# Optimization experiments

Hardware: AMD Instinct MI355X
Metric: run time of the kernel (lower is better)

## Reference

```python
import jax, jax.numpy as jnp
import numpy as np

NUM_LANDMARKS = 1024  # must equal seq_len for the source einsum/pinv shapes to be consistent


def setup_inputs() -> dict:
    key = jax.random.key(0)
    ks = jax.random.split(key, 9)
    B, S, D = 4, 1024, 768
    s = 1.0 / np.sqrt(D)  # ~torch Linear default init scale
    return {
        "q": jax.random.normal(ks[0], (B, S, D), jnp.float32),
        "k": jax.random.normal(ks[1], (B, S, D), jnp.float32),
        "v": jax.random.normal(ks[2], (B, S, D), jnp.float32),
        "Wq": jax.random.normal(ks[3], (D, D), jnp.float32) * s,
        "bq": jax.random.normal(ks[4], (D,), jnp.float32) * s,
        "Wk": jax.random.normal(ks[5], (D, D), jnp.float32) * s,
        "bk": jax.random.normal(ks[6], (D,), jnp.float32) * s,
        "Wv": jax.random.normal(ks[7], (D, D), jnp.float32) * s,
        "bv": jax.random.normal(ks[8], (D,), jnp.float32) * s,
    }


def reference(q, k, v, Wq, bq, Wk, bk, Wv, bv):
    B, S, D = q.shape
    m = NUM_LANDMARKS
    # projections + row softmax over feature dim (as in source; note: self.scale is unused there)
    qp = jax.nn.softmax(q @ Wq + bq, axis=-1)            # [B,S,D]
    kp = jax.nn.softmax(k @ Wk + bk, axis=-1)            # [B,S,D]
    vp = v @ Wv + bv                                     # [B,S,D]
    # landmark mean pooling (with m == S this is the identity pooling)
    q_land = qp.reshape(B, m, -1, D).mean(axis=-2)       # [B,m,D]
    k_land = kp.reshape(B, m, -1, D).mean(axis=-2)       # [B,m,D]
    kernel_1 = jnp.einsum('bqd,bkd->bqk', qp, k_land)    # [B,S,m]
    kernel_2 = jnp.einsum('bkd,bld->bkl', k_land, kp)    # [B,m,S]
    kernel_3 = kp * vp                                   # [B,S,D]
    kernel_2_inv = jnp.linalg.pinv(kernel_2)             # [B,S,m] (== [B,m,S] since m==S)
    out = jnp.einsum('bqk,bkl,bld->bqd', kernel_1, kernel_2_inv, kernel_3)
    return out
```

## Files before the change

### kernel.cpp

```cpp
#include <hip/hip_runtime.h>
#include <cstdint>


#define NB 4
#define SS 1024
#define DD 768

static const long PB = (long)SS * DD;
static const long GB = (long)DD * DD;
static const long SZ_P = (long)NB * PB;
static const long SZ_G = (long)NB * GB;

__global__ __launch_bounds__(256)
void gemm_f32(int M, int N, int K,
              const float* __restrict__ A, long sA,
              const float* __restrict__ Bm, long sB,
              float* __restrict__ C, long sC,
              const float* __restrict__ Dm, long sD,
              const float* __restrict__ bias,
              float alpha, float beta)
{
    const int b = blockIdx.z;
    const float* Ab = A + (long)b * sA;
    const float* Bb = Bm + (long)b * sB;
    float*       Cb = C + (long)b * sC;
    const float* Db = Dm ? (Dm + (long)b * sD) : nullptr;

    __shared__ float As[16][68];
    __shared__ float Bs[16][68];

    const int tid = threadIdx.x;
    const int tx = tid & 15, ty = tid >> 4;
    const int row0 = blockIdx.y * 64, col0 = blockIdx.x * 64;

    const int lar = tid >> 2;
    const int lak = (tid & 3) << 2;
    const int lbc = (tid & 15) << 2;
    const int lbk = tid >> 4;

    float acc[4][4] = {};

    for (int k0 = 0; k0 < K; k0 += 16) {
        float4 av = *(const float4*)(Ab + (long)(row0 + lar) * K + (k0 + lak));
        float4 bv = *(const float4*)(Bb + (long)(k0 + lbk) * N + (col0 + lbc));
        As[lak + 0][lar] = av.x;
        As[lak + 1][lar] = av.y;
        As[lak + 2][lar] = av.z;
        As[lak + 3][lar] = av.w;
        *(float4*)(&Bs[lbk][lbc]) = bv;
        __syncthreads();
#pragma unroll
        for (int kk = 0; kk < 16; ++kk) {
            float4 a4 = *(const float4*)(&As[kk][ty << 2]);
            float4 b4 = *(const float4*)(&Bs[kk][tx << 2]);
            float ar[4] = {a4.x, a4.y, a4.z, a4.w};
            float br[4] = {b4.x, b4.y, b4.z, b4.w};
#pragma unroll
            for (int i = 0; i < 4; ++i)
#pragma unroll
                for (int j = 0; j < 4; ++j)
                    acc[i][j] = fmaf(ar[i], br[j], acc[i][j]);
        }
        __syncthreads();
    }

#pragma unroll
    for (int i = 0; i < 4; ++i) {
        const int r = row0 + (ty << 2) + i;
#pragma unroll
        for (int j = 0; j < 4; ++j) {
            const int c = col0 + (tx << 2) + j;
            float vv = alpha * acc[i][j];
            if (Db)   vv += beta * Db[(long)r * N + c];
            if (bias) vv += bias[c];
            Cb[(long)r * N + c] = vv;
        }
    }
}

__global__ __launch_bounds__(256)
void gram_gm(const float* __restrict__ KP, const float* __restrict__ VP,
             float* __restrict__ G, float* __restrict__ Mo)
{
    const int b = blockIdx.z;
    const float* Kb = KP + (long)b * PB;
    const float* Vb = VP + (long)b * PB;
    float* Gb = G  + (long)b * GB;
    float* Mb = Mo + (long)b * GB;

    __shared__ float As[16][68];
    __shared__ float Bs[16][68];
    __shared__ float Cs[16][68];

    const int tid = threadIdx.x;
    const int tx = tid & 15, ty = tid >> 4;
    const int i0 = blockIdx.y * 64, j0 = blockIdx.x * 64;
    const int lc = (tid & 15) << 2;
    const int ls = tid >> 4;

    float accG[4][4] = {};
    float accM[4][4] = {};

    for (int s0 = 0; s0 < SS; s0 += 16) {
        const long ro = (long)(s0 + ls) * DD;
        float4 ka = *(const float4*)(Kb + ro + i0 + lc);
        float4 kb = *(const float4*)(Kb + ro + j0 + lc);
        float4 vb = *(const float4*)(Vb + ro + j0 + lc);
        *(float4*)(&As[ls][lc]) = ka;
        *(float4*)(&Bs[ls][lc]) = kb;
        float4 kv = make_float4(kb.x * vb.x, kb.y * vb.y, kb.z * vb.z, kb.w * vb.w);
        *(float4*)(&Cs[ls][lc]) = kv;
        __syncthreads();
#pragma unroll
        for (int ss = 0; ss < 16; ++ss) {
            float4 a4 = *(const float4*)(&As[ss][ty << 2]);
            float4 b4 = *(const float4*)(&Bs[ss][tx << 2]);
            float4 c4 = *(const float4*)(&Cs[ss][tx << 2]);
            float ar[4] = {a4.x, a4.y, a4.z, a4.w};
            float br[4] = {b4.x, b4.y, b4.z, b4.w};
            float cr[4] = {c4.x, c4.y, c4.z, c4.w};
#pragma unroll
            for (int i = 0; i < 4; ++i)
#pragma unroll
                for (int j = 0; j < 4; ++j) {
                    accG[i][j] = fmaf(ar[i], br[j], accG[i][j]);
                    accM[i][j] = fmaf(ar[i], cr[j], accM[i][j]);
                }
        }
        __syncthreads();
    }

#pragma unroll
    for (int i = 0; i < 4; ++i) {
        const int r = i0 + (ty << 2) + i;
#pragma unroll
        for (int j = 0; j < 4; ++j) {
            const int c = j0 + (tx << 2) + j;
            Gb[(long)r * DD + c] = accG[i][j];
            Mb[(long)r * DD + c] = accM[i][j];
        }
    }
}

__global__ __launch_bounds__(256)
void softmax_rows(float* __restrict__ P)
{
    const int row  = blockIdx.x * 4 + (threadIdx.x >> 6);
    const int lane = threadIdx.x & 63;
    float* rp = P + (long)row * DD;
    float v[12];
    float mx = -3.4e38f;
#pragma unroll
    for (int i = 0; i < 12; ++i) { v[i] = rp[lane + (i << 6)]; mx = fmaxf(mx, v[i]); }
#pragma unroll
    for (int off = 32; off > 0; off >>= 1) mx = fmaxf(mx, __shfl_xor(mx, off, 64));
    float sum = 0.f;
#pragma unroll
    for (int i = 0; i < 12; ++i) { v[i] = expf(v[i] - mx); sum += v[i]; }
#pragma unroll
    for (int off = 32; off > 0; off >>= 1) sum += __shfl_xor(sum, off, 64);
#pragma unroll
    for (int i = 0; i < 12; ++i) rp[lane + (i << 6)] = v[i] / sum;
}

__global__ __launch_bounds__(256)
void power_iter(const float* __restrict__ G, float* __restrict__ scal)
{
    const int b = blockIdx.x;
    const float* Gb = G + (long)b * GB;
    __shared__ __align__(16) float v[DD];
    __shared__ float w[DD];
    __shared__ float red[256];
    const int t = threadIdx.x;
    for (int i = t; i < DD; i += 256) v[i] = 1.0f;
    __syncthreads();
    float lam = 1.f;
    for (int it = 0; it < 12; ++it) {
        for (int r = t; r < DD; r += 256) {
            const float4* gr = (const float4*)(Gb + (long)r * DD);
            float s = 0.f;
            for (int c4 = 0; c4 < DD / 4; ++c4) {
                float4 g4 = gr[c4];
                float4 vv = *(const float4*)(&v[c4 << 2]);
                s = fmaf(g4.x, vv.x, s); s = fmaf(g4.y, vv.y, s);
                s = fmaf(g4.z, vv.z, s); s = fmaf(g4.w, vv.w, s);
            }
            w[r] = s;
        }
        __syncthreads();
        float ps = 0.f;
        for (int i = t; i < DD; i += 256) ps += w[i] * w[i];
        red[t] = ps; __syncthreads();
        for (int off = 128; off > 0; off >>= 1) {
            if (t < off) red[t] += red[t + off];
            __syncthreads();
        }
        lam = sqrtf(red[0]);
        const float inv = 1.0f / lam;
        __syncthreads();
        for (int i = t; i < DD; i += 256) v[i] = w[i] * inv;
        __syncthreads();
    }
    if (t == 0) {
        scal[b]     = lam;
        scal[4 + b] = 1.220703125e-3f * lam;
        scal[8 + b] = 1.0f / lam;
    }
}

__global__ __launch_bounds__(256)
void mat_sign_init(const float* __restrict__ G, float* __restrict__ X,
                   const float* __restrict__ scal)
{
    const long idx = (long)blockIdx.x * 256 + threadIdx.x;
    if (idx >= SZ_G) return;
    const int b = (int)(idx / GB);
    const long rem = idx % GB;
    const int r = (int)(rem / DD), c = (int)(rem % DD);
    float g = G[idx];
    if (r == c) g -= scal[4 + b];
    X[idx] = g * scal[8 + b];
}

__global__ __launch_bounds__(256)
void mat_proj_init(const float* __restrict__ Sg, float* __restrict__ X,
                   const float* __restrict__ scal)
{
    const long idx = (long)blockIdx.x * 256 + threadIdx.x;
    if (idx >= SZ_G) return;
    const int b = (int)(idx / GB);
    const long rem = idx % GB;
    const int r = (int)(rem / DD), c = (int)(rem % DD);
    float s = Sg[idx];
    if (r == c) s += 1.0f;
    X[idx] = s * 0.5f * scal[8 + b];
}

extern "C" void kernel_launch(void* const* d_in, const int* in_sizes, int n_in,
                              void* d_out, int out_size, void* d_ws, size_t ws_size,
                              hipStream_t stream)
{
    (void)in_sizes; (void)n_in; (void)out_size; (void)ws_size;
    const float* q  = (const float*)d_in[0];
    const float* k  = (const float*)d_in[1];
    const float* v  = (const float*)d_in[2];
    const float* Wq = (const float*)d_in[3];
    const float* bq = (const float*)d_in[4];
    const float* Wk = (const float*)d_in[5];
    const float* bk = (const float*)d_in[6];
    const float* Wv = (const float*)d_in[7];
    const float* bv = (const float*)d_in[8];
    float* out = (float*)d_out;

    float* ws = (float*)d_ws;
    float* QP   = ws;
    float* KP   = QP + SZ_P;
    float* VP   = KP + SZ_P;
    float* G    = VP + SZ_P;
    float* Mm   = G  + SZ_G;
    float* T1   = Mm + SZ_G;
    float* scal = T1 + SZ_G;
    float* X  = KP;
    float* T2 = VP;

    const dim3 blk(256);
    const dim3 gP(DD / 64, SS / 64, NB);
    const dim3 gG(DD / 64, DD / 64, NB);
    const dim3 gE((unsigned)((SZ_G + 255) / 256));
    const float* nf = nullptr;

    hipLaunchKernelGGL(gemm_f32, gP, blk, 0, stream, SS, DD, DD, q, PB, Wq, 0L, QP, PB, nf, 0L, bq, 1.0f, 0.0f);
    hipLaunchKernelGGL(gemm_f32, gP, blk, 0, stream, SS, DD, DD, k, PB, Wk, 0L, KP, PB, nf, 0L, bk, 1.0f, 0.0f);
    hipLaunchKernelGGL(gemm_f32, gP, blk, 0, stream, SS, DD, DD, v, PB, Wv, 0L, VP, PB, nf, 0L, bv, 1.0f, 0.0f);

    hipLaunchKernelGGL(softmax_rows, dim3(NB * SS / 4), blk, 0, stream, QP);
    hipLaunchKernelGGL(softmax_rows, dim3(NB * SS / 4), blk, 0, stream, KP);

    hipLaunchKernelGGL(gram_gm, gG, blk, 0, stream, KP, VP, G, Mm);

    hipLaunchKernelGGL(power_iter, dim3(NB), blk, 0, stream, G, scal);

    hipLaunchKernelGGL(mat_sign_init, gE, blk, 0, stream, G, X, scal);
    float* sp = X; float* op = T2;
    for (int it = 0; it < 28; ++it) {
        const float a  = (it < 20) ? 2.4f   : 1.5f;
        const float bb = (it < 20) ? 2.048f : 0.5f;
        hipLaunchKernelGGL(gemm_f32, gG, blk, 0, stream, DD, DD, DD, sp, GB, sp, GB, T1, GB, nf, 0L, nf, 1.0f, 0.0f);
        hipLaunchKernelGGL(gemm_f32, gG, blk, 0, stream, DD, DD, DD, sp, GB, T1, GB, op, GB, sp, GB, nf, -bb, a);
        float* t = sp; sp = op; op = t;
    }

    hipLaunchKernelGGL(mat_proj_init, gE, blk, 0, stream, sp, op, scal);
    { float* t = sp; sp = op; op = t; }
    for (int it = 0; it < 14; ++it) {
        hipLaunchKernelGGL(gemm_f32, gG, blk, 0, stream, DD, DD, DD, G, GB, sp, GB, T1, GB, nf, 0L, nf, 1.0f, 0.0f);
        hipLaunchKernelGGL(gemm_f32, gG, blk, 0, stream, DD, DD, DD, sp, GB, T1, GB, op, GB, sp, GB, nf, -1.0f, 2.0f);
        float* t = sp; sp = op; op = t;
    }

    hipLaunchKernelGGL(gemm_f32, gG, blk, 0, stream, DD, DD, DD, sp, GB, Mm, GB, T1, GB, nf, 0L, nf, 1.0f, 0.0f);
    hipLaunchKernelGGL(gemm_f32, gP, blk, 0, stream, SS, DD, DD, QP, PB, T1, GB, out, PB, nf, 0L, nf, 1.0f, 0.0f);
}
```

Before: 7.464 ms.

## Use 128x128 GEMM tiles with split-K and restructure sign/projection iterations

Replaces the 64x64 GEMM with a 128x128 tile, 8x8-per-thread kernel and adds a split-K path with a separate reduction for the small 768x768 iterative GEMMs, so more blocks are in flight. The fused Gram kernel becomes a kv_mul elementwise pass followed by two transposed-A GEMMs. The single-block power iteration is replaced by parallel matrix-vector kernels run for fewer steps. The sign iteration's last 8 cubic steps are replaced by 4 quintic steps, and the projection Newton loop is cut from 14 to 13 iterations. Split-K adds extra partial-sum traffic and launches, and the numerical changes (fewer power steps, quintic steps, different scaling) may affect accuracy.

```diff
diff --git a/kernel.cpp b/kernel.cpp
--- a/kernel.cpp
+++ b/kernel.cpp
@@ -5,141 +5,138 @@
 #define NB 4
 #define SS 1024
 #define DD 768
-
-static const long PB = (long)SS * DD;
-static const long GB = (long)DD * DD;
+#define BK 16
+
+static const long PB   = (long)SS * DD;
+static const long GB   = (long)DD * DD;
 static const long SZ_P = (long)NB * PB;
 static const long SZ_G = (long)NB * GB;
-
-__global__ __launch_bounds__(256)
-void gemm_f32(int M, int N, int K,
-              const float* __restrict__ A, long sA,
-              const float* __restrict__ Bm, long sB,
-              float* __restrict__ C, long sC,
-              const float* __restrict__ Dm, long sD,
-              const float* __restrict__ bias,
-              float alpha, float beta)
-{
-    const int b = blockIdx.z;
-    const float* Ab = A + (long)b * sA;
-    const float* Bb = Bm + (long)b * sB;
-    float*       Cb = C + (long)b * sC;
-    const float* Db = Dm ? (Dm + (long)b * sD) : nullptr;
-
-    __shared__ float As[16][68];
-    __shared__ float Bs[16][68];
-
-    const int tid = threadIdx.x;
-    const int tx = tid & 15, ty = tid >> 4;
-    const int row0 = blockIdx.y * 64, col0 = blockIdx.x * 64;
-
-    const int lar = tid >> 2;
-    const int lak = (tid & 3) << 2;
-    const int lbc = (tid & 15) << 2;
-    const int lbk = tid >> 4;
-
-    float acc[4][4] = {};
-
-    for (int k0 = 0; k0 < K; k0 += 16) {
-        float4 av = *(const float4*)(Ab + (long)(row0 + lar) * K + (k0 + lak));
-        float4 bv = *(const float4*)(Bb + (long)(k0 + lbk) * N + (col0 + lbc));
-        As[lak + 0][lar] = av.x;
-        As[lak + 1][lar] = av.y;
-        As[lak + 2][lar] = av.z;
-        As[lak + 3][lar] = av.w;
-        *(float4*)(&Bs[lbk][lbc]) = bv;
+#define RTOL 1.220703125e-3f
+
+template<bool TA, bool SPLITK>
+__global__ __launch_bounds__(256, 3)
+void gemm8(int M, int N, int K, int nsplitLg,
+           const float* __restrict__ A, long sA,
+           const float* __restrict__ B, long sB,
+           float* __restrict__ C, long sC, long partStride,
+           const float* __restrict__ Dm, long sD,
+           const float* __restrict__ bias,
+           float alpha, float beta)
+{
+    const int z   = blockIdx.z;
+    const int bb  = z >> nsplitLg;
+    const int sp  = z & ((1 << nsplitLg) - 1);
+    const int Ks  = K >> nsplitLg;
+    const int kbeg = sp * Ks;
+
+    const float* Ab = A + (long)bb * sA;
+    const float* Bb = B + (long)bb * sB;
+
+    __shared__ float As[BK][132];
+    __shared__ float Bs[BK][132];
+
+    const int t  = threadIdx.x;
+    const int tx = t & 15, ty = t >> 4;
+    const int row0 = blockIdx.y * 128, col0 = blockIdx.x * 128;
+
+    const int a_row = t >> 1;
+    const int a_kq  = (t & 1) << 3;
+    const int l_k   = t >> 5;
+    const int l_q   = (t & 31) << 2;
+
+    float acc[8][8] = {};
+
+    for (int k0 = kbeg; k0 < kbeg + Ks; k0 += BK) {
+        if (TA) {
+            float4 v0 = *(const float4*)(Ab + (long)(k0 + l_k) * M + row0 + l_q);
+            float4 v1 = *(const float4*)(Ab + (long)(k0 + l_k + 8) * M + row0 + l_q);
+            *(float4*)(&As[l_k][l_q])     = v0;
+            *(float4*)(&As[l_k + 8][l_q]) = v1;
+        } else {
+            float4 v0 = *(const float4*)(Ab + (long)(row0 + a_row) * K + k0 + a_kq);
+            float4 v1 = *(const float4*)(Ab + (long)(row0 + a_row) * K + k0 + a_kq + 4);
+            As[a_kq + 0][a_row] = v0.x; As[a_kq + 1][a_row] = v0.y;
+            As[a_kq + 2][a_row] = v0.z; As[a_kq + 3][a_row] = v0.w;
+            As[a_kq + 4][a_row] = v1.x; As[a_kq + 5][a_row] = v1.y;
+            As[a_kq + 6][a_row] = v1.z; As[a_kq + 7][a_row] = v1.w;
+        }
+        {
+            float4 v0 = *(const float4*)(Bb + (long)(k0 + l_k) * N + col0 + l_q);
+            float4 v1 = *(const float4*)(Bb + (long)(k0 + l_k + 8) * N + col0 + l_q);
+            *(float4*)(&Bs[l_k][l_q])     = v0;
+            *(float4*)(&Bs[l_k + 8][l_q]) = v1;
+        }
         __syncthreads();
 #pragma unroll
-        for (int kk = 0; kk < 16; ++kk) {
-            float4 a4 = *(const float4*)(&As[kk][ty << 2]);
-            float4 b4 = *(const float4*)(&Bs[kk][tx << 2]);
-            float ar[4] = {a4.x, a4.y, a4.z, a4.w};
-            float br[4] = {b4.x, b4.y, b4.z, b4.w};
-#pragma unroll
-            for (int i = 0; i < 4; ++i)
-#pragma unroll
-                for (int j = 0; j < 4; ++j)
+        for (int kk = 0; kk < BK; ++kk) {
+            float4 a0 = *(const float4*)(&As[kk][ty << 3]);
+            float4 a1 = *(const float4*)(&As[kk][(ty << 3) + 4]);
+            float4 b0 = *(const float4*)(&Bs[kk][tx << 3]);
+            float4 b1 = *(const float4*)(&Bs[kk][(tx << 3) + 4]);
+            float ar[8] = {a0.x,a0.y,a0.z,a0.w,a1.x,a1.y,a1.z,a1.w};
+            float br[8] = {b0.x,b0.y,b0.z,b0.w,b1.x,b1.y,b1.z,b1.w};
+#pragma unroll
+            for (int i = 0; i < 8; ++i)
+#pragma unroll
+                for (int j = 0; j < 8; ++j)
                     acc[i][j] = fmaf(ar[i], br[j], acc[i][j]);
         }
         __syncthreads();
     }
 
-#pragma unroll
-    for (int i = 0; i < 4; ++i) {
-        const int r = row0 + (ty << 2) + i;
-#pragma unroll
-        for (int j = 0; j < 4; ++j) {
-            const int c = col0 + (tx << 2) + j;
-            float vv = alpha * acc[i][j];
-            if (Db)   vv += beta * Db[(long)r * N + c];
-            if (bias) vv += bias[c];
-            Cb[(long)r * N + c] = vv;
-        }
-    }
-}
-
-__global__ __launch_bounds__(256)
-void gram_gm(const float* __restrict__ KP, const float* __restrict__ VP,
-             float* __restrict__ G, float* __restrict__ Mo)
-{
-    const int b = blockIdx.z;
-    const float* Kb = KP + (long)b * PB;
-    const float* Vb = VP + (long)b * PB;
-    float* Gb = G  + (long)b * GB;
-    float* Mb = Mo + (long)b * GB;
-
-    __shared__ float As[16][68];
-    __shared__ float Bs[16][68];
-    __shared__ float Cs[16][68];
-
-    const int tid = threadIdx.x;
-    const int tx = tid & 15, ty = tid >> 4;
-    const int i0 = blockIdx.y * 64, j0 = blockIdx.x * 64;
-    const int lc = (tid & 15) << 2;
-    const int ls = tid >> 4;
-
-    float accG[4][4] = {};
-    float accM[4][4] = {};
-
-    for (int s0 = 0; s0 < SS; s0 += 16) {
-        const long ro = (long)(s0 + ls) * DD;
-        float4 ka = *(const float4*)(Kb + ro + i0 + lc);
-        float4 kb = *(const float4*)(Kb + ro + j0 + lc);
-        float4 vb = *(const float4*)(Vb + ro + j0 + lc);
-        *(float4*)(&As[ls][lc]) = ka;
-        *(float4*)(&Bs[ls][lc]) = kb;
-        float4 kv = make_float4(kb.x * vb.x, kb.y * vb.y, kb.z * vb.z, kb.w * vb.w);
-        *(float4*)(&Cs[ls][lc]) = kv;
-        __syncthreads();
-#pragma unroll
-        for (int ss = 0; ss < 16; ++ss) {
-            float4 a4 = *(const float4*)(&As[ss][ty << 2]);
-            float4 b4 = *(const float4*)(&Bs[ss][tx << 2]);
-            float4 c4 = *(const float4*)(&Cs[ss][tx << 2]);
-            float ar[4] = {a4.x, a4.y, a4.z, a4.w};
-            float br[4] = {b4.x, b4.y, b4.z, b4.w};
-            float cr[4] = {c4.x, c4.y, c4.z, c4.w};
-#pragma unroll
-            for (int i = 0; i < 4; ++i)
-#pragma unroll
-                for (int j = 0; j < 4; ++j) {
-                    accG[i][j] = fmaf(ar[i], br[j], accG[i][j]);
-                    accM[i][j] = fmaf(ar[i], cr[j], accM[i][j]);
-                }
-        }
-        __syncthreads();
-    }
-
-#pragma unroll
-    for (int i = 0; i < 4; ++i) {
-        const int r = i0 + (ty << 2) + i;
-#pragma unroll
-        for (int j = 0; j < 4; ++j) {
-            const int c = j0 + (tx << 2) + j;
-            Gb[(long)r * DD + c] = accG[i][j];
-            Mb[(long)r * DD + c] = accM[i][j];
-        }
-    }
+    if (SPLITK) {
+        float* P = C + (long)sp * partStride + (long)bb * sC;
+#pragma unroll
+        for (int i = 0; i < 8; ++i) {
+            const long ro = (long)(row0 + (ty << 3) + i) * N + col0 + (tx << 3);
+            *(float4*)(P + ro)     = make_float4(acc[i][0], acc[i][1], acc[i][2], acc[i][3]);
+            *(float4*)(P + ro + 4) = make_float4(acc[i][4], acc[i][5], acc[i][6], acc[i][7]);
+        }
+    } else {
+        float* Cb = C + (long)bb * sC;
+        const float* Db = Dm ? Dm + (long)bb * sD : nullptr;
+#pragma unroll
+        for (int i = 0; i < 8; ++i) {
+            const int r = row0 + (ty << 3) + i;
+            const long ro = (long)r * N + col0 + (tx << 3);
+            float4 o0 = make_float4(alpha*acc[i][0], alpha*acc[i][1], alpha*acc[i][2], alpha*acc[i][3]);
+            float4 o1 = make_float4(alpha*acc[i][4], alpha*acc[i][5], alpha*acc[i][6], alpha*acc[i][7]);
+            if (Db) {
+                float4 d0 = *(const float4*)(Db + ro);
+                float4 d1 = *(const float4*)(Db + ro + 4);
+                o0.x += beta*d0.x; o0.y += beta*d0.y; o0.z += beta*d0.z; o0.w += beta*d0.w;
+                o1.x += beta*d1.x; o1.y += beta*d1.y; o1.z += beta*d1.z; o1.w += beta*d1.w;
+            }
+            if (bias) {
+                float4 s0 = *(const float4*)(bias + col0 + (tx << 3));
+                float4 s1 = *(const float4*)(bias + col0 + (tx << 3) + 4);
+                o0.x += s0.x; o0.y += s0.y; o0.z += s0.z; o0.w += s0.w;
+                o1.x += s1.x; o1.y += s1.y; o1.z += s1.z; o1.w += s1.w;
+            }
+            *(float4*)(Cb + ro)     = o0;
+            *(float4*)(Cb + ro + 4) = o1;
+        }
+    }
+}
+
+__global__ __launch_bounds__(256)
+void reduceN(const float* __restrict__ P, long partStride, int nparts,
+             float* __restrict__ C, const float* __restrict__ Dm,
+             float alpha, float beta, long n4)
+{
+    const long i = (long)blockIdx.x * 256 + threadIdx.x;
+    if (i >= n4) return;
+    float4 s = ((const float4*)P)[i];
+    for (int p = 1; p < nparts; ++p) {
+        float4 v = ((const float4*)(P + (long)p * partStride))[i];
+        s.x += v.x; s.y += v.y; s.z += v.z; s.w += v.w;
+    }
+    float4 o = make_float4(alpha*s.x, alpha*s.y, alpha*s.z, alpha*s.w);
+    if (Dm) {
+        float4 d = ((const float4*)Dm)[i];
+        o.x += beta*d.x; o.y += beta*d.y; o.z += beta*d.z; o.w += beta*d.w;
+    }
+    ((float4*)C)[i] = o;
 }
 
 __global__ __launch_bounds__(256)
@@ -164,47 +161,67 @@
 }
 
 __global__ __launch_bounds__(256)
-void power_iter(const float* __restrict__ G, float* __restrict__ scal)
-{
-    const int b = blockIdx.x;
-    const float* Gb = G + (long)b * GB;
-    __shared__ __align__(16) float v[DD];
-    __shared__ float w[DD];
+void kv_mul(const float* __restrict__ KP, float* __restrict__ VP)
+{
+    const long i = (long)blockIdx.x * 256 + threadIdx.x;
+    if (i < SZ_P) VP[i] *= KP[i];
+}
+
+__global__ __launch_bounds__(256)
+void init_ones(float* __restrict__ v)
+{
+    const int i = blockIdx.x * 256 + threadIdx.x;
+    if (i < NB * DD) v[i] = 1.0f;
+}
+
+__global__ __launch_bounds__(256)
+void mv768(const float* __restrict__ G, const float* __restrict__ vin,
+           float* __restrict__ vout)
+{
+    const int b = blockIdx.y;
+    const int r = blockIdx.x * 4 + (threadIdx.x >> 6);
+    const int l = threadIdx.x & 63;
+    const float* Gr = G + (long)b * GB + (long)r * DD;
+    const float* vb = vin + b * DD;
+    float s = 0.f;
+#pragma unroll
+    for (int j = 0; j < 3; ++j) {
+        float4 g4 = *(const float4*)(Gr + (l << 2) + j * 256);
+        float4 v4 = *(const float4*)(vb + (l << 2) + j * 256);
+        s = fmaf(g4.x, v4.x, s); s = fmaf(g4.y, v4.y, s);
+        s = fmaf(g4.z, v4.z, s); s = fmaf(g4.w, v4.w, s);
+    }
+#pragma unroll
+    for (int off = 32; off > 0; off >>= 1) s += __shfl_xor(s, off, 64);
+    if (l == 0) vout[b * DD + r] = s;
+}
+
+__global__ __launch_bounds__(256)
+void lam_tau(const float* __restrict__ vprev, const float* __restrict__ vcur,
+             float* __restrict__ scal)
+{
     __shared__ float red[256];
     const int t = threadIdx.x;
-    for (int i = t; i < DD; i += 256) v[i] = 1.0f;
-    __syncthreads();
-    float lam = 1.f;
-    for (int it = 0; it < 12; ++it) {
-        for (int r = t; r < DD; r += 256) {
-            const float4* gr = (const float4*)(Gb + (long)r * DD);
-            float s = 0.f;
-            for (int c4 = 0; c4 < DD / 4; ++c4) {
-                float4 g4 = gr[c4];
-                float4 vv = *(const float4*)(&v[c4 << 2]);
-                s = fmaf(g4.x, vv.x, s); s = fmaf(g4.y, vv.y, s);
-                s = fmaf(g4.z, vv.z, s); s = fmaf(g4.w, vv.w, s);
-            }
-            w[r] = s;
+    for (int b = 0; b < NB; ++b) {
+        float sp = 0.f, sc = 0.f;
+        for (int i = t; i < DD; i += 256) {
+            float a = vprev[b * DD + i], c = vcur[b * DD + i];
+            sp = fmaf(a, a, sp); sc = fmaf(c, c, sc);
+        }
+        red[t] = sp; __syncthreads();
+        for (int o = 128; o > 0; o >>= 1) { if (t < o) red[t] += red[t + o]; __syncthreads(); }
+        const float np = red[0]; __syncthreads();
+        red[t] = sc; __syncthreads();
+        for (int o = 128; o > 0; o >>= 1) { if (t < o) red[t] += red[t + o]; __syncthreads(); }
+        const float nc = red[0]; __syncthreads();
+        if (t == 0) {
+            const float lam = sqrtf(nc / np);
+            scal[b]      = lam;
+            scal[4 + b]  = RTOL * lam;
+            scal[8 + b]  = 1.0f / lam;
+            scal[12 + b] = 1.0f / (lam * (1.0f + RTOL));
         }
         __syncthreads();
-        float ps = 0.f;
-        for (int i = t; i < DD; i += 256) ps += w[i] * w[i];
-        red[t] = ps; __syncthreads();
-        for (int off = 128; off > 0; off >>= 1) {
-            if (t < off) red[t] += red[t + off];
-            __syncthreads();
-        }
-        lam = sqrtf(red[0]);
-        const float inv = 1.0f / lam;
-        __syncthreads();
-        for (int i = t; i < DD; i += 256) v[i] = w[i] * inv;
-        __syncthreads();
-    }
-    if (t == 0) {
-        scal[b]     = lam;
-        scal[4 + b] = 1.220703125e-3f * lam;
-        scal[8 + b] = 1.0f / lam;
     }
 }
 
@@ -233,14 +250,27 @@
     const int r = (int)(rem / DD), c = (int)(rem % DD);
     float s = Sg[idx];
     if (r == c) s += 1.0f;
-    X[idx] = s * 0.5f * scal[8 + b];
+    X[idx] = s * scal[12 + b];
+}
+
+__global__ __launch_bounds__(256)
+void quintic_u(const float* __restrict__ T, const float* __restrict__ T2,
+               float* __restrict__ U)
+{
+    const long idx = (long)blockIdx.x * 256 + threadIdx.x;
+    if (idx >= SZ_G) return;
+    const long rem = idx % GB;
+    const int r = (int)(rem / DD), c = (int)(rem % DD);
+    float u = -1.25f * T[idx] + 0.375f * T2[idx];
+    if (r == c) u += 1.875f;
+    U[idx] = u;
 }
 
 extern "C" void kernel_launch(void* const* d_in, const int* in_sizes, int n_in,
                               void* d_out, int out_size, void* d_ws, size_t ws_size,
                               hipStream_t stream)
 {
-    (void)in_sizes; (void)n_in; (void)out_size; (void)ws_size;
+    (void)in_sizes; (void)n_in; (void)out_size;
     const float* q  = (const float*)d_in[0];
     const float* k  = (const float*)d_in[1];
     const float* v  = (const float*)d_in[2];
@@ -253,51 +283,95 @@
     float* out = (float*)d_out;
 
     float* ws = (float*)d_ws;
-    float* QP   = ws;
-    float* KP   = QP + SZ_P;
-    float* VP   = KP + SZ_P;
-    float* G    = VP + SZ_P;
-    float* Mm   = G  + SZ_G;
-    float* T1   = Mm + SZ_G;
-    float* scal = T1 + SZ_G;
-    float* X  = KP;
-    float* T2 = VP;
+    float* QP    = ws;
+    float* KP    = QP + SZ_P;
+    float* VP    = KP + SZ_P;
+    float* G     = VP + SZ_P;
+    float* Mm    = G  + SZ_G;
+    float* Yb    = Mm + SZ_G;
+    float* Ub    = Yb + SZ_G;
+    float* vb0   = Ub + SZ_G;
+    float* vb1   = vb0 + NB * DD;
+    float* scal  = vb1 + NB * DD;
+    float* parts = scal + 16;
+    const size_t need_split = (size_t)((parts + 4 * SZ_G) - ws) * sizeof(float);
+    const bool split = ws_size >= need_split;
 
     const dim3 blk(256);
-    const dim3 gP(DD / 64, SS / 64, NB);
-    const dim3 gG(DD / 64, DD / 64, NB);
+    const dim3 gP(6, 8, NB);
+    const dim3 gG(6, 6, NB);
+    const dim3 gGs(6, 6, NB * 4);
     const dim3 gE((unsigned)((SZ_G + 255) / 256));
     const float* nf = nullptr;
-
-    hipLaunchKernelGGL(gemm_f32, gP, blk, 0, stream, SS, DD, DD, q, PB, Wq, 0L, QP, PB, nf, 0L, bq, 1.0f, 0.0f);
-    hipLaunchKernelGGL(gemm_f32, gP, blk, 0, stream, SS, DD, DD, k, PB, Wk, 0L, KP, PB, nf, 0L, bk, 1.0f, 0.0f);
-    hipLaunchKernelGGL(gemm_f32, gP, blk, 0, stream, SS, DD, DD, v, PB, Wv, 0L, VP, PB, nf, 0L, bv, 1.0f, 0.0f);
+    const long n4 = SZ_G / 4;
+    const unsigned gR = (unsigned)((n4 + 255) / 256);
+
+    auto iterGemm = [&](const float* A_, const float* B_, float* out_,
+                        const float* Dm_, float alpha_, float beta_) {
+        if (split) {
+            hipLaunchKernelGGL((gemm8<false, true>), gGs, blk, 0, stream,
+                               DD, DD, DD, 2, A_, GB, B_, GB,
+                               parts, GB, (long)NB * GB, nf, 0L, nf, 1.0f, 0.0f);
+            hipLaunchKernelGGL(reduceN, dim3(gR), blk, 0, stream,
+                               parts, (long)NB * GB, 4, out_, Dm_, alpha_, beta_, n4);
+        } else {
+            hipLaunchKernelGGL((gemm8<false, false>), gG, blk, 0, stream,
+                               DD, DD, DD, 0, A_, GB, B_, GB,
+                               out_, GB, 0L, Dm_, GB, nf, alpha_, beta_);
+        }
+    };
+
+    hipLaunchKernelGGL((gemm8<false, false>), gP, blk, 0, stream,
+                       SS, DD, DD, 0, q, PB, Wq, 0L, QP, PB, 0L, nf, 0L, bq, 1.0f, 0.0f);
+    hipLaunchKernelGGL((gemm8<false, false>), gP, blk, 0, stream,
+                       SS, DD, DD, 0, k, PB, Wk, 0L, KP, PB, 0L, nf, 0L, bk, 1.0f, 0.0f);
+    hipLaunchKernelGGL((gemm8<false, false>), gP, blk, 0, stream,
+                       SS, DD, DD, 0, v, PB, Wv, 0L, VP, PB, 0L, nf, 0L, bv, 1.0f, 0.0f);
 
     hipLaunchKernelGGL(softmax_rows, dim3(NB * SS / 4), blk, 0, stream, QP);
     hipLaunchKernelGGL(softmax_rows, dim3(NB * SS / 4), blk, 0, stream, KP);
 
-    hipLaunchKernelGGL(gram_gm, gG, blk, 0, stream, KP, VP, G, Mm);
-
-    hipLaunchKernelGGL(power_iter, dim3(NB), blk, 0, stream, G, scal);
-
-    hipLaunchKernelGGL(mat_sign_init, gE, blk, 0, stream, G, X, scal);
-    float* sp = X; float* op = T2;
-    for (int it = 0; it < 28; ++it) {
-        const float a  = (it < 20) ? 2.4f   : 1.5f;
-        const float bb = (it < 20) ? 2.048f : 0.5f;
-        hipLaunchKernelGGL(gemm_f32, gG, blk, 0, stream, DD, DD, DD, sp, GB, sp, GB, T1, GB, nf, 0L, nf, 1.0f, 0.0f);
-        hipLaunchKernelGGL(gemm_f32, gG, blk, 0, stream, DD, DD, DD, sp, GB, T1, GB, op, GB, sp, GB, nf, -bb, a);
-        float* t = sp; sp = op; op = t;
-    }
-
-    hipLaunchKernelGGL(mat_proj_init, gE, blk, 0, stream, sp, op, scal);
-    { float* t = sp; sp = op; op = t; }
-    for (int it = 0; it < 14; ++it) {
-        hipLaunchKernelGGL(gemm_f32, gG, blk, 0, stream, DD, DD, DD, G, GB, sp, GB, T1, GB, nf, 0L, nf, 1.0f, 0.0f);
-        hipLaunchKernelGGL(gemm_f32, gG, blk, 0, stream, DD, DD, DD, sp, GB, T1, GB, op, GB, sp, GB, nf, -1.0f, 2.0f);
-        float* t = sp; sp = op; op = t;
-    }
-
-    hipLaunchKernelGGL(gemm_f32, gG, blk, 0, stream, DD, DD, DD, sp, GB, Mm, GB, T1, GB, nf, 0L, nf, 1.0f, 0.0f);
-    hipLaunchKernelGGL(gemm_f32, gP, blk, 0, stream, SS, DD, DD, QP, PB, T1, GB, out, PB, nf, 0L, nf, 1.0f, 0.0f);
-}
+    hipLaunchKernelGGL(kv_mul, dim3((unsigned)((SZ_P + 255) / 256)), blk, 0, stream, KP, VP);
+    hipLaunchKernelGGL((gemm8<true, false>), gG, blk, 0, stream,
+                       DD, DD, SS, 0, KP, PB, KP, PB, G, GB, 0L, nf, 0L, nf, 1.0f, 0.0f);
+    hipLaunchKernelGGL((gemm8<true, false>), gG, blk, 0, stream,
+                       DD, DD, SS, 0, KP, PB, VP, PB, Mm, GB, 0L, nf, 0L, nf, 1.0f, 0.0f);
+
+    hipLaunchKernelGGL(init_ones, dim3(12), blk, 0, stream, vb0);
+    for (int it = 0; it < 4; ++it) {
+        hipLaunchKernelGGL(mv768, dim3(192, NB), blk, 0, stream, G, vb0, vb1);
+        hipLaunchKernelGGL(mv768, dim3(192, NB), blk, 0, stream, G, vb1, vb0);
+    }
+    hipLaunchKernelGGL(lam_tau, dim3(1), blk, 0, stream, vb1, vb0, scal);
+
+    float* cur = KP;
+    float* oth = Yb;
+    float* t1  = VP;
+    float* t2  = Ub;
+    hipLaunchKernelGGL(mat_sign_init, gE, blk, 0, stream, G, cur, scal);
+    for (int it = 0; it < 20; ++it) {
+        iterGemm(cur, cur, t1, nf, 1.0f, 0.0f);
+        iterGemm(cur, t1, oth, cur, -2.048f, 2.4f);
+        float* tmp = cur; cur = oth; oth = tmp;
+    }
+    for (int it = 0; it < 4; ++it) {
+        iterGemm(cur, cur, t1, nf, 1.0f, 0.0f);
+        iterGemm(t1, t1, t2, nf, 1.0f, 0.0f);
+        hipLaunchKernelGGL(quintic_u, gE, blk, 0, stream, t1, t2, t1);
+        iterGemm(cur, t1, oth, nf, 1.0f, 0.0f);
+        float* tmp = cur; cur = oth; oth = tmp;
+    }
+
+    hipLaunchKernelGGL(mat_proj_init, gE, blk, 0, stream, cur, oth, scal);
+    { float* tmp = cur; cur = oth; oth = tmp; }
+    for (int it = 0; it < 13; ++it) {
+        iterGemm(G, cur, t1, nf, 1.0f, 0.0f);
+        iterGemm(cur, t1, oth, cur, -1.0f, 2.0f);
+        float* tmp = cur; cur = oth; oth = tmp;
+    }
+
+    hipLaunchKernelGGL((gemm8<false, false>), gG, blk, 0, stream,
+                       DD, DD, DD, 0, cur, GB, Mm, GB, t1, GB, 0L, nf, 0L, nf, 1.0f, 0.0f);
+    hipLaunchKernelGGL((gemm8<false, false>), gP, blk, 0, stream,
+                       SS, DD, DD, 0, QP, PB, t1, GB, out, PB, 0L, nf, 0L, nf, 1.0f, 0.0f);
+}
```

Result: faster. 6.322 ms (-15.3%).
